# Optimization experiments

Hardware: AMD Instinct MI355X
Metric: run time of the kernel (lower is better)

## Reference

```python
import jax, jax.numpy as jnp
import numpy as np

HEAD_K_DIM = 128  # linear_key_head_dim (not derivable from weight shapes alone)
EPS_NORM = 1e-6


def _l2norm(x, eps=1e-6):
    return x * jax.lax.rsqrt(jnp.sum(x * x, axis=-1, keepdims=True) + eps)


def setup_inputs() -> dict:
    key = jax.random.key(0)
    ks = jax.random.split(key, 9)
    B, S, H = 2, 1024, 2048
    Hv, Hk, Dk, Dv, K = 32, 16, 128, 128, 4
    key_dim, value_dim = Hk * Dk, Hv * Dv
    C = 2 * key_dim + value_dim  # conv_dim = 8192
    s = 0.02
    return {
        "hidden_states": jax.random.normal(ks[0], (B, S, H), jnp.float32),
        "conv_state": jnp.zeros((B, C, K - 1), jnp.float32),
        "recurrent_state": jnp.zeros((B, Hv, Dk, Dv), jnp.float32),
        "W_qkv": (jax.random.normal(ks[1], (C, H)) * s).astype(jnp.float32),
        "W_z": (jax.random.normal(ks[2], (value_dim, H)) * s).astype(jnp.float32),
        "W_b": (jax.random.normal(ks[3], (Hv, H)) * s).astype(jnp.float32),
        "W_a": (jax.random.normal(ks[4], (Hv, H)) * s).astype(jnp.float32),
        "conv_w": (jax.random.normal(ks[5], (C, K)) * s).astype(jnp.float32),
        "dt_bias": jnp.ones((Hv,), jnp.float32),
        "A_log": jnp.log(jax.random.uniform(ks[6], (Hv,), jnp.float32, 1e-3, 16.0)),
        "norm_weight": jnp.ones((Dv,), jnp.float32),
        "W_out": (jax.random.normal(ks[7], (H, value_dim)) * s).astype(jnp.float32),
    }


def reference(hidden_states, conv_state, recurrent_state, W_qkv, W_z, W_b, W_a,
              conv_w, dt_bias, A_log, norm_weight, W_out):
    B, S, H = hidden_states.shape
    Hv = dt_bias.shape[0]
    Dv = norm_weight.shape[0]
    C, K = conv_w.shape
    value_dim = Hv * Dv
    key_dim = (C - value_dim) // 2
    Dk = HEAD_K_DIM
    Hk = key_dim // Dk

    # input projections
    mixed_qkv = jnp.einsum('bsh,ch->bcs', hidden_states, W_qkv)  # (B, C, S)
    z = hidden_states @ W_z.T                                    # (B, S, value_dim)
    b = hidden_states @ W_b.T                                    # (B, S, Hv)
    a = hidden_states @ W_a.T                                    # (B, S, Hv)

    # causal depthwise conv over time with cached prefix state
    padded = jnp.concatenate([conv_state, mixed_qkv], axis=-1)   # (B, C, K-1+S)
    conv_out = sum(padded[:, :, k:k + S] * conv_w[:, k][None, :, None]
                   for k in range(K))                            # (B, C, S)
    conv_state_new = padded[:, :, -(K - 1):]
    mixed = jnp.swapaxes(jax.nn.silu(conv_out), 1, 2)            # (B, S, C)

    q = mixed[..., :key_dim].reshape(B, S, Hk, Dk)
    k = mixed[..., key_dim:2 * key_dim].reshape(B, S, Hk, Dk)
    v = mixed[..., 2 * key_dim:].reshape(B, S, Hv, Dv)

    beta = jax.nn.sigmoid(b)                                     # (B, S, Hv)
    g = -jnp.exp(A_log) * jax.nn.softplus(a + dt_bias)           # (B, S, Hv)

    rep = Hv // Hk
    if rep > 1:
        q = jnp.repeat(q, rep, axis=2)
        k = jnp.repeat(k, rep, axis=2)

    scale = Dk ** (-0.5)
    q = _l2norm(q) * scale
    k = _l2norm(k)

    # time-leading for scan: (S, B, Hv, ...)
    qT, kT, vT = (jnp.moveaxis(x, 1, 0) for x in (q, k, v))
    gT, betaT = jnp.moveaxis(g, 1, 0), jnp.moveaxis(beta, 1, 0)

    def step(state, xs):
        q_t, k_t, v_t, g_t, beta_t = xs
        state = state * jnp.exp(g_t)[..., None, None]            # decay
        kv_mem = jnp.einsum('bhk,bhkv->bhv', k_t, state)         # read
        delta = (v_t - kv_mem) * beta_t[..., None]               # correction
        state = state + jnp.einsum('bhk,bhv->bhkv', k_t, delta)  # write
        out_t = jnp.einsum('bhk,bhkv->bhv', q_t, state)          # readout
        return state, out_t

    final_state, outs = jax.lax.scan(step, recurrent_state.astype(jnp.float32),
                                     (qT, kT, vT, gT, betaT))
    core = jnp.moveaxis(outs, 0, 1)                              # (B, S, Hv, Dv)

    # gated RMS norm per value head
    var = jnp.mean(core * core, axis=-1, keepdims=True)
    xn = core * jax.lax.rsqrt(var + EPS_NORM) * norm_weight
    gated = xn * jax.nn.silu(z.reshape(B, S, Hv, Dv))

    output = gated.reshape(B, S, value_dim) @ W_out.T            # (B, S, H)
    return output, conv_state_new, final_state
```

## Files before the change

### kernel.cpp

```cpp
#include <hip/hip_runtime.h>
#include <cstdint>
#include <cstddef>

#define B_ 2
#define S_ 1024
#define H_ 2048
#define HV_ 32
#define HK_ 16
#define DK_ 128
#define DV_ 128
#define CC_ 8192
#define KEYDIM_ 2048
#define VALDIM_ 4096
#define NC_ 16
#define CS_ 64
#define NBIG 12416
#define NBIGP 12544

typedef __attribute__((ext_vector_type(8))) short bf16x8;
typedef __attribute__((ext_vector_type(4))) float f32x4;

__device__ __forceinline__ ushort f2bf_rne(float x) {
  union { float f; uint32_t u; } c; c.f = x;
  uint32_t u = c.u + 0x7FFFu + ((c.u >> 16) & 1u);
  return (ushort)(u >> 16);
}

__device__ __forceinline__ void gld16(const void* g, void* l) {
  __builtin_amdgcn_global_load_lds(
      (const __attribute__((address_space(1))) void*)g,
      (__attribute__((address_space(3))) void*)l, 16, 0, 0);
}

__global__ void f2bf_kernel(const float* __restrict__ in, ushort* __restrict__ out, int n) {
  int i = (blockIdx.x * 256 + threadIdx.x) * 4;
  if (i >= n) return;
  float4 v = *(const float4*)(in + i);
  ushort4 o;
  o.x = f2bf_rne(v.x); o.y = f2bf_rne(v.y);
  o.z = f2bf_rne(v.z); o.w = f2bf_rne(v.w);
  *(ushort4*)(out + i) = o;
}

__global__ void wcat_kernel(const float* __restrict__ Wqkv, const float* __restrict__ Wz,
                            const float* __restrict__ Wb, const float* __restrict__ Wa,
                            ushort* __restrict__ out) {
  int i = (blockIdx.x * 256 + threadIdx.x) * 4;
  if (i >= NBIGP * H_) return;
  int n = i >> 11;
  int k = i & (H_ - 1);
  float4 v = make_float4(0.f, 0.f, 0.f, 0.f);
  if (n < 8192)       v = *(const float4*)(Wqkv + (size_t)n * H_ + k);
  else if (n < 12288) v = *(const float4*)(Wz + (size_t)(n - 8192) * H_ + k);
  else if (n < 12320) v = *(const float4*)(Wb + (size_t)(n - 12288) * H_ + k);
  else if (n < 12352) v = *(const float4*)(Wa + (size_t)(n - 12320) * H_ + k);
  ushort4 o;
  o.x = f2bf_rne(v.x); o.y = f2bf_rne(v.y);
  o.z = f2bf_rne(v.z); o.w = f2bf_rne(v.w);
  *(ushort4*)(out + i) = o;
}

#define MEMF() asm volatile("" ::: "memory")
#define VMW(n) asm volatile("s_waitcnt vmcnt(" #n ")" ::: "memory")
#define BARR() do { __builtin_amdgcn_s_barrier(); MEMF(); } while (0)

#define ST(P, SHM, RG, o, kq) do {                                  \
    gld16((P) + (kq),      &SHM[o][((RG) * 2 + 0) * 512]);          \
    gld16((P) + (kq) + 32, &SHM[o][((RG) * 2 + 1) * 512]);          \
  } while (0)

#define LDA(ah, c) do { _Pragma("unroll")                                            \
    for (int i_ = 0; i_ < 4; i_++) { _Pragma("unroll")                               \
      for (int h_ = 0; h_ < 2; h_++)                                                 \
        aF[i_ * 2 + h_] = *(const bf16x8*)(                                          \
            &sAm[c][((wm * 8 + (ah) * 4 + i_) * 2 + h_) * 512 + lane * 8]); } } while (0)

#define LDB(dst, bh, c) do { _Pragma("unroll")                                       \
    for (int j_ = 0; j_ < 2; j_++) { _Pragma("unroll")                               \
      for (int h_ = 0; h_ < 2; h_++)                                                 \
        dst[j_ * 2 + h_] = *(const bf16x8*)(                                         \
            &sBm[c][((wn * 4 + (bh) * 2 + j_) * 2 + h_) * 512 + lane * 8]); } } while (0)

#define MM(ah, bh, bsrc) do {                                                        \
    __builtin_amdgcn_s_setprio(1);                                                   \
    _Pragma("unroll") for (int h_ = 0; h_ < 2; h_++)                                 \
    _Pragma("unroll") for (int i_ = 0; i_ < 4; i_++)                                 \
    _Pragma("unroll") for (int j_ = 0; j_ < 2; j_++)                                 \
      acc[(ah) * 4 + i_][(bh) * 2 + j_] = __builtin_amdgcn_mfma_f32_16x16x32_bf16(   \
          aF[i_ * 2 + h_], bsrc[j_ * 2 + h_], acc[(ah) * 4 + i_][(bh) * 2 + j_],     \
          0, 0, 0);                                                                  \
    __builtin_amdgcn_s_setprio(0);                                                   \
  } while (0)

__global__ __launch_bounds__(512, 2) void gemm256_8ph(
    const ushort* __restrict__ A, const ushort* __restrict__ B,
    float* __restrict__ C, int Ns, int K)
{
  __shared__ ushort sAm[2][16384];
  __shared__ ushort sBm[2][16384];

  const int t = threadIdx.x;
  const int wave = t >> 6, lane = t & 63;
  const int wm = wave >> 2, wn = wave & 3;
  const int l15 = lane & 15, l4 = lane >> 4;
  const int mt = blockIdx.x, nt = blockIdx.y;

  const int rgS0 = (wave & 3) + (wave >> 2) * 8;
  const int rgS3 = rgS0 + 4;
  const int rgS1 = (wave & 1) + (wave >> 1) * 4;
  const int rgS2 = rgS1 + 2;

  const ushort* aP0 = A + (size_t)(mt * 256 + rgS0 * 16 + l15) * K + l4 * 8;
  const ushort* aP1 = A + (size_t)(mt * 256 + rgS3 * 16 + l15) * K + l4 * 8;
  const ushort* bP0 = B + (size_t)(nt * 256 + rgS1 * 16 + l15) * K + l4 * 8;
  const ushort* bP1 = B + (size_t)(nt * 256 + rgS2 * 16 + l15) * K + l4 * 8;

  f32x4 acc[8][4];
  #pragma unroll
  for (int i = 0; i < 8; i++)
    #pragma unroll
    for (int j = 0; j < 4; j++)
      #pragma unroll
      for (int r = 0; r < 4; r++) acc[i][j][r] = 0.f;

  bf16x8 aF[8], bF0[4], bF1[4];

  ST(aP0, sAm, rgS0, 0, 0); MEMF();
  ST(bP0, sBm, rgS1, 0, 0); MEMF();
  ST(bP1, sBm, rgS2, 0, 0); MEMF();
  ST(aP1, sAm, rgS3, 0, 0); MEMF();

  const int NT = K >> 6;
  for (int tt = 0; tt < NT - 1; tt++) {
    const int c = tt & 1, o = c ^ 1;
    const int kq = (tt + 1) << 6;
    VMW(4); BARR();
    ST(aP0, sAm, rgS0, o, kq);
    LDA(0, c); LDB(bF0, 0, c);
    MM(0, 0, bF0);
    VMW(4); BARR();
    ST(bP0, sBm, rgS1, o, kq);
    LDB(bF1, 1, c);
    MM(0, 1, bF1);
    VMW(4); BARR();
    ST(bP1, sBm, rgS2, o, kq);
    LDA(1, c);
    MM(1, 1, bF1);
    MEMF();
    ST(aP1, sAm, rgS3, o, kq);
    MM(1, 0, bF0);
  }
  {
    const int c = (NT - 1) & 1;
    VMW(4); BARR();
    LDA(0, c); LDB(bF0, 0, c);
    MM(0, 0, bF0);
    VMW(2); BARR();
    LDB(bF1, 1, c);
    MM(0, 1, bF1);
    VMW(0); BARR();
    LDA(1, c);
    MM(1, 1, bF1);
    MM(1, 0, bF0);
  }

  #pragma unroll
  for (int mf = 0; mf < 8; mf++) {
    const int row0 = mt * 256 + wm * 128 + mf * 16 + l4 * 4;
    #pragma unroll
    for (int nf = 0; nf < 4; nf++) {
      const int col = nt * 256 + wn * 64 + nf * 16 + l15;
      if (col < Ns) {
        #pragma unroll
        for (int r = 0; r < 4; r++)
          C[(size_t)(row0 + r) * Ns + col] = acc[mf][nf][r];
      }
    }
  }
}

__device__ __forceinline__ void stage_tile(
    const ushort* aS0, const ushort* aS1, const ushort* bS0, const ushort* bS1,
    ushort* ldsA, ushort* ldsB, int wave, int k0)
{
  #pragma unroll
  for (int h = 0; h < 2; h++) {
    gld16(aS0 + k0 + h * 32, ldsA + h * 4096 + (wave * 2 + 0) * 512);
    gld16(aS1 + k0 + h * 32, ldsA + h * 4096 + (wave * 2 + 1) * 512);
    gld16(bS0 + k0 + h * 32, ldsB + h * 4096 + (wave * 2 + 0) * 512);
    gld16(bS1 + k0 + h * 32, ldsB + h * 4096 + (wave * 2 + 1) * 512);
  }
}

__global__ __launch_bounds__(256) void gemm_bf16_nt(
    const ushort* __restrict__ A, const ushort* __restrict__ B,
    float* __restrict__ C, int M, int N, int K)
{
  __shared__ ushort sL[2][2][8192];
  int t = threadIdx.x;
  int wave = t >> 6, lane = t & 63;
  int wm = wave >> 1, wn = wave & 1;
  int lrow = lane & 15, quad = lane >> 4;
  int mt = blockIdx.x, nt = blockIdx.y;

  f32x4 acc[4][4];
  #pragma unroll
  for (int i = 0; i < 4; i++)
    #pragma unroll
    for (int j = 0; j < 4; j++)
      #pragma unroll
      for (int r = 0; r < 4; r++) acc[i][j][r] = 0.f;

  const ushort* aS0 = A + (size_t)(mt * 128 + (wave * 2 + 0) * 16 + lrow) * K + quad * 8;
  const ushort* aS1 = A + (size_t)(mt * 128 + (wave * 2 + 1) * 16 + lrow) * K + quad * 8;
  const ushort* bS0 = B + (size_t)(nt * 128 + (wave * 2 + 0) * 16 + lrow) * K + quad * 8;
  const ushort* bS1 = B + (size_t)(nt * 128 + (wave * 2 + 1) * 16 + lrow) * K + quad * 8;

  stage_tile(aS0, aS1, bS0, bS1, &sL[0][0][0], &sL[0][1][0], wave, 0);
  __syncthreads();

  const int NK = K >> 6;
  for (int it = 0; it < NK; it++) {
    if (it + 1 < NK)
      stage_tile(aS0, aS1, bS0, bS1,
                 &sL[(it + 1) & 1][0][0], &sL[(it + 1) & 1][1][0],
                 wave, (it + 1) * 64);
    const ushort* bufA = &sL[it & 1][0][0];
    const ushort* bufB = &sL[it & 1][1][0];
    #pragma unroll
    for (int h = 0; h < 2; h++) {
      bf16x8 af[4], bfr[4];
      #pragma unroll
      for (int i = 0; i < 4; i++)
        af[i] = *(const bf16x8*)(bufA + h * 4096 + (wm * 4 + i) * 512 + lane * 8);
      #pragma unroll
      for (int j = 0; j < 4; j++)
        bfr[j] = *(const bf16x8*)(bufB + h * 4096 + (wn * 4 + j) * 512 + lane * 8);
      #pragma unroll
      for (int i = 0; i < 4; i++)
        #pragma unroll
        for (int j = 0; j < 4; j++)
          acc[i][j] = __builtin_amdgcn_mfma_f32_16x16x32_bf16(af[i], bfr[j], acc[i][j], 0, 0, 0);
    }
    __syncthreads();
  }

  #pragma unroll
  for (int i = 0; i < 4; i++) {
    int m_base = mt * 128 + wm * 64 + i * 16 + quad * 4;
    #pragma unroll
    for (int j = 0; j < 4; j++) {
      int n = nt * 128 + wn * 64 + j * 16 + lrow;
      #pragma unroll
      for (int rr = 0; rr < 4; rr++)
        C[(size_t)(m_base + rr) * N + n] = acc[i][j][rr];
    }
  }
}

__global__ void convstate_kernel(const float* __restrict__ Cbig,
                                 float* __restrict__ out)
{
  int idx = blockIdx.x * blockDim.x + threadIdx.x;
  if (idx >= B_ * CC_ * 3) return;
  int j = idx % 3;
  int c = (idx / 3) % CC_;
  int b = idx / (3 * CC_);
  out[idx] = Cbig[((size_t)(b * S_ + (S_ - 3 + j))) * NBIG + c];
}

__global__ __launch_bounds__(128) void prep_qkv(
    const float* __restrict__ Cbig, const float* __restrict__ conv_state,
    const float* __restrict__ conv_w,
    float* __restrict__ Qn, float* __restrict__ Kn, float* __restrict__ Vb)
{
  int group = blockIdx.x, s = blockIdx.y, b = blockIdx.z;
  int t = threadIdx.x;
  int c = group * 128 + t;
  float acc = 0.f;
  #pragma unroll
  for (int kk = 0; kk < 4; kk++) {
    int sp = s - 3 + kk;
    float x = (sp < 0) ? conv_state[((size_t)(b * CC_ + c)) * 3 + (3 + sp)]
                       : Cbig[((size_t)(b * S_ + sp)) * NBIG + c];
    acc += conv_w[c * 4 + kk] * x;
  }
  float val = acc / (1.f + __expf(-acc));

  if (group < 32) {
    __shared__ float red2[2];
    float p = val * val;
    #pragma unroll
    for (int off = 32; off > 0; off >>= 1) p += __shfl_xor(p, off);
    if ((t & 63) == 0) red2[t >> 6] = p;
    __syncthreads();
    float r = rsqrtf(red2[0] + red2[1] + 1e-6f);
    if (group < 16) {
      r *= 0.08838834764831845f;
      Qn[(((size_t)(b * HK_ + group)) * S_ + s) * DK_ + t] = val * r;
    } else {
      Kn[(((size_t)(b * HK_ + (group - 16))) * S_ + s) * DK_ + t] = val * r;
    }
  } else {
    Vb[(((size_t)(b * HV_ + (group - 32))) * S_ + s) * DV_ + t] = val;
  }
}

__global__ void prep_gb(const float* __restrict__ Cbig,
                        const float* __restrict__ A_log, const float* __restrict__ dt_bias,
                        float* __restrict__ g_buf, float* __restrict__ beta_buf)
{
  int idx = blockIdx.x * blockDim.x + threadIdx.x;
  if (idx >= B_ * HV_ * S_) return;
  int s = idx & (S_ - 1);
  int hv = (idx >> 10) & 31;
  int b = idx >> 15;
  float bv = Cbig[((size_t)(b * S_ + s)) * NBIG + 12288 + hv];
  float av = Cbig[((size_t)(b * S_ + s)) * NBIG + 12320 + hv];
  float x = av + dt_bias[hv];
  float sp = (x > 20.f) ? x : log1pf(__expf(x));
  g_buf[idx] = -__expf(A_log[hv]) * sp;
  beta_buf[idx] = 1.f / (1.f + __expf(-bv));
}

__device__ __forceinline__ int swf4(int r, int f) { return r * 32 + (f ^ (r & 31)); }
__device__ __forceinline__ int swf1(int r, int k) {
  return r * 128 + 4 * ((k >> 2) ^ (r & 31)) + (k & 3);
}

__global__ __launch_bounds__(256) void cp_kernel(
    const float* __restrict__ Qn, const float* __restrict__ Kn,
    const float* __restrict__ Vb,
    const float* __restrict__ g_buf, const float* __restrict__ beta_buf,
    float* __restrict__ G_buf, float* __restrict__ M_buf,
    float* __restrict__ KcD, float* __restrict__ D0p)
{
  __shared__ float sK[64 * 128];
  __shared__ float sX[32 * 128];
  __shared__ float sT[64 * 64];
  float* sG  = sT;
  float* sBe = sT + 64;
  float* sA  = sX;
  float* tTw = sX;
  float* tTb = sX;
  float4* sK4 = (float4*)sK;
  float4* sX4 = (float4*)sX;

  const int ch = blockIdx.x;
  const int bh = ch / NC_, c = ch % NC_;
  const int b = bh >> 5, hv = bh & 31, hk = hv >> 1;
  const int s0 = c * CS_;
  const int t = threadIdx.x;
  const size_t gOff = (size_t)bh * S_ + s0;

  float Gw0 = 0.f, Bw0 = 0.f;
  if (t < 64) {
    float gi = g_buf[gOff + t];
    Gw0 = gi;
    #pragma unroll
    for (int off = 1; off < 64; off <<= 1) {
      float o = __shfl_up(Gw0, off);
      if (t >= off) Gw0 += o;
    }
    G_buf[gOff + t] = Gw0;
    sG[t] = Gw0;
    Bw0 = beta_buf[gOff + t];
    sBe[t] = Bw0;
  }
  {
    const float4* src = (const float4*)(Kn + ((size_t)(b * HK_ + hk) * S_ + s0) * DK_);
    #pragma unroll
    for (int u = 0; u < 8; u++) {
      int idx = u * 256 + t;
      sK4[swf4(idx >> 5, idx & 31)] = src[idx];
    }
  }
  __syncthreads();

  const float4* qsrc = (const float4*)(Qn + ((size_t)(b * HK_ + hk) * S_ + s0) * DK_);
  {
    int ti2 = t >> 4, tj = t & 15;
    for (int h = 0; h < 2; h++) {
      #pragma unroll
      for (int u = 0; u < 4; u++) {
        int idx = u * 256 + t;
        sX4[swf4(idx >> 5, idx & 31)] = qsrc[h * 1024 + idx];
      }
      __syncthreads();
      float accM[2][4];
      #pragma unroll
      for (int a = 0; a < 2; a++)
        #pragma unroll
        for (int e = 0; e < 4; e++) accM[a][e] = 0.f;
      for (int k4 = 0; k4 < 32; k4++) {
        float4 qv[2], kv[4];
        qv[0] = sX4[swf4(ti2, k4)];
        qv[1] = sX4[swf4(ti2 + 16, k4)];
        #pragma unroll
        for (int e = 0; e < 4; e++) kv[e] = sK4[swf4(tj + 16 * e, k4)];
        #pragma unroll
        for (int a = 0; a < 2; a++)
          #pragma unroll
          for (int e = 0; e < 4; e++)
            accM[a][e] += qv[a].x * kv[e].x + qv[a].y * kv[e].y +
                          qv[a].z * kv[e].z + qv[a].w * kv[e].w;
      }
      #pragma unroll
      for (int a = 0; a < 2; a++) {
        int iG = h * 32 + ti2 + 16 * a;
        float Gi = sG[iG];
        #pragma unroll
        for (int e = 0; e < 4; e++) {
          int j = tj + 16 * e;
          float m = (j <= iG) ? __expf(Gi - sG[j]) * accM[a][e] : 0.f;
          M_buf[(size_t)ch * 4096 + iG * 64 + j] = m;
        }
      }
      __syncthreads();
    }
  }

  {
    int ti = t >> 4, tj = t & 15;
    float accA[4][4];
    #pragma unroll
    for (int a = 0; a < 4; a++)
      #pragma unroll
      for (int e = 0; e < 4; e++) accA[a][e] = 0.f;
    for (int k4 = 0; k4 < 32; k4++) {
      float4 ki[4], kj[4];
      #pragma unroll
      for (int e = 0; e < 4; e++) {
        ki[e] = sK4[swf4(ti + 16 * e, k4)];
        kj[e] = sK4[swf4(tj + 16 * e, k4)];
      }
      #pragma unroll
      for (int a = 0; a < 4; a++)
        #pragma unroll
        for (int e = 0; e < 4; e++)
          accA[a][e] += ki[a].x * kj[e].x + ki[a].y * kj[e].y +
                        ki[a].z * kj[e].z + ki[a].w * kj[e].w;
    }
    float resA[4][4];
    #pragma unroll
    for (int a = 0; a < 4; a++) {
      int i = ti + 16 * a;
      float Gi = sG[i], Bi = sBe[i];
      #pragma unroll
      for (int e = 0; e < 4; e++) {
        int j = tj + 16 * e;
        resA[a][e] = (j < i) ? Bi * __expf(Gi - sG[j]) * accA[a][e] : 0.f;
      }
    }
    __syncthreads();
    #pragma unroll
    for (int a = 0; a < 4; a++)
      #pragma unroll
      for (int e = 0; e < 4; e++)
        sA[(ti + 16 * a) * 64 + (tj + 16 * e)] = resA[a][e];
  }
  __syncthreads();

  if (t < 64) {
    sT[t] = (t == 0) ? 1.f : 0.f;
    for (int i = 1; i < 64; i++) {
      float acc = 0.f;
      for (int j = 0; j < i; j++) acc += sA[i * 64 + j] * sT[j * 64 + t];
      sT[i * 64 + t] = ((t == i) ? 1.f : 0.f) - acc;
    }
    float w = Bw0 * __expf(Gw0);
    for (int j = 0; j < 64; j++) {
      float wj = __shfl(w, j);
      tTw[j * 64 + t] = sT[t * 64 + j] * wj;
    }
  }
  __syncthreads();

  {
    int i04 = t >> 4, tk = t & 15;
    float accK[4][8];
    #pragma unroll
    for (int r = 0; r < 4; r++)
      #pragma unroll
      for (int u = 0; u < 8; u++) accK[r][u] = 0.f;
    for (int j = 0; j < 64; j++) {
      float4 tw = ((float4*)tTw)[j * 16 + i04];
      #pragma unroll
      for (int u = 0; u < 8; u++) {
        float kv = sK[swf1(j, tk + 16 * u)];
        accK[0][u] += tw.x * kv; accK[1][u] += tw.y * kv;
        accK[2][u] += tw.z * kv; accK[3][u] += tw.w * kv;
      }
    }
    size_t base = (size_t)ch * NBIG;
    #pragma unroll
    for (int r = 0; r < 4; r++)
      #pragma unroll
      for (int u = 0; u < 8; u++)
        KcD[base + (i04 * 4 + r) * 128 + tk + 16 * u] = accK[r][u];
  }
  __syncthreads();

  if (t < 64) {
    for (int j = 0; j < 64; j++) {
      float bj = __shfl(Bw0, j);
      tTb[j * 64 + t] = sT[t * 64 + j] * bj;
    }
  }
  {
    const float4* src = (const float4*)(Vb + ((size_t)bh * S_ + s0) * DV_);
    #pragma unroll
    for (int u = 0; u < 8; u++) {
      int idx = u * 256 + t;
      sK4[swf4(idx >> 5, idx & 31)] = src[idx];
    }
  }
  __syncthreads();

  {
    int i04 = t >> 4, tv_ = t & 15;
    float accD[4][8];
    #pragma unroll
    for (int r = 0; r < 4; r++)
      #pragma unroll
      for (int u = 0; u < 8; u++) accD[r][u] = 0.f;
    for (int j = 0; j < 64; j++) {
      float4 tb = ((float4*)tTb)[j * 16 + i04];
      #pragma unroll
      for (int u = 0; u < 8; u++) {
        float vv = sK[swf1(j, tv_ + 16 * u)];
        accD[0][u] += tb.x * vv; accD[1][u] += tb.y * vv;
        accD[2][u] += tb.z * vv; accD[3][u] += tb.w * vv;
      }
    }
    size_t base = (size_t)ch * NBIG;
    #pragma unroll
    for (int r = 0; r < 4; r++)
      #pragma unroll
      for (int u = 0; u < 8; u++)
        D0p[base + (i04 * 4 + r) * 128 + tv_ + 16 * u] = accD[r][u];
  }
}

__global__ __launch_bounds__(256) void phaseb_kernel(
    const float* __restrict__ rec_state, const float* __restrict__ Qn,
    const float* __restrict__ Kn, const float* __restrict__ G_buf,
    float* __restrict__ KcD, const float* __restrict__ D0p,
    float* __restrict__ Oq_buf, float* __restrict__ final_state)
{
  __shared__ float sS[128 * 32];
  __shared__ float sKT[128 * 64];
  __shared__ float sQT[128 * 64];
  __shared__ float sD[64 * 32];

  const int blk = blockIdx.x;
  const int bh = (blk & 7) | ((blk >> 5) << 3);
  const int vq = (blk >> 3) & 3;
  const int b = bh >> 5, hv = bh & 31, hk = hv >> 1;
  const int t = threadIdx.x;
  const int vbase = vq * 32;
  const float* gG = G_buf + (size_t)bh * S_;

  #pragma unroll
  for (int u = 0; u < 4; u++) {
    int idx = u * 256 + t;
    int k = idx >> 3;
    int v4 = (idx & 7) * 4;
    *(float4*)(&sS[k * 32 + v4]) =
        *(const float4*)(&rec_state[((size_t)bh * 128 + k) * 128 + vbase + v4]);
  }
  __syncthreads();

  const int si = t & 63, skq = t >> 6;
  const int ti = t >> 3;
  const int tv = t & 7;
  const int tk = t >> 3;

  for (int c = 0; c < NC_; c++) {
    const size_t ch = (size_t)bh * NC_ + c;
    const int s0 = c * CS_;
    const float GC = gG[s0 + 63];
    const float eGC = __expf(GC);

    {
      float eGi = __expf(gG[s0 + si]);
      const float* kcRow = KcD + ch * NBIG + si * 128 + skq * 32;
      const float* qRow  = Qn + ((size_t)(b * HK_ + hk) * S_ + s0 + si) * DK_ + skq * 32;
      #pragma unroll
      for (int u = 0; u < 8; u++) {
        float4 kc = *(const float4*)(kcRow + u * 4);
        float4 qv = *(const float4*)(qRow + u * 4);
        int kk = skq * 32 + u * 4;
        sKT[(kk + 0) * 64 + si] = kc.x; sKT[(kk + 1) * 64 + si] = kc.y;
        sKT[(kk + 2) * 64 + si] = kc.z; sKT[(kk + 3) * 64 + si] = kc.w;
        sQT[(kk + 0) * 64 + si] = qv.x * eGi; sQT[(kk + 1) * 64 + si] = qv.y * eGi;
        sQT[(kk + 2) * 64 + si] = qv.z * eGi; sQT[(kk + 3) * 64 + si] = qv.w * eGi;
      }
    }
    __syncthreads();

    {
      float accD[2][4], accO[2][4];
      #pragma unroll
      for (int r = 0; r < 2; r++) {
        float4 d0 = *(const float4*)(&D0p[ch * NBIG + (size_t)(ti * 2 + r) * 128 + vbase + tv * 4]);
        accD[r][0] = d0.x; accD[r][1] = d0.y; accD[r][2] = d0.z; accD[r][3] = d0.w;
        accO[r][0] = accO[r][1] = accO[r][2] = accO[r][3] = 0.f;
      }
      for (int k = 0; k < 128; k++) {
        float2 kc = *(const float2*)(&sKT[k * 64 + ti * 2]);
        float2 qb = *(const float2*)(&sQT[k * 64 + ti * 2]);
        float4 sv = *(const float4*)(&sS[k * 32 + tv * 4]);
        accD[0][0] -= kc.x * sv.x; accD[0][1] -= kc.x * sv.y;
        accD[0][2] -= kc.x * sv.z; accD[0][3] -= kc.x * sv.w;
        accD[1][0] -= kc.y * sv.x; accD[1][1] -= kc.y * sv.y;
        accD[1][2] -= kc.y * sv.z; accD[1][3] -= kc.y * sv.w;
        accO[0][0] += qb.x * sv.x; accO[0][1] += qb.x * sv.y;
        accO[0][2] += qb.x * sv.z; accO[0][3] += qb.x * sv.w;
        accO[1][0] += qb.y * sv.x; accO[1][1] += qb.y * sv.y;
        accO[1][2] += qb.y * sv.z; accO[1][3] += qb.y * sv.w;
      }
      #pragma unroll
      for (int r = 0; r < 2; r++) {
        int i = ti * 2 + r;
        float4 dv = make_float4(accD[r][0], accD[r][1], accD[r][2], accD[r][3]);
        float4 ov = make_float4(accO[r][0], accO[r][1], accO[r][2], accO[r][3]);
        *(float4*)(&sD[i * 32 + tv * 4]) = dv;
        *(float4*)(&KcD[ch * NBIG + (size_t)i * 128 + vbase + tv * 4]) = dv;
        *(float4*)(&Oq_buf[ch * 8192 + (size_t)i * 128 + vbase + tv * 4]) = ov;
      }
    }
    __syncthreads();

    {
      float sc = __expf(GC - gG[s0 + si]);
      const float* kRow = Kn + ((size_t)(b * HK_ + hk) * S_ + s0 + si) * DK_ + skq * 32;
      #pragma unroll
      for (int u = 0; u < 8; u++) {
        float4 x = *(const float4*)(kRow + u * 4);
        x.x *= sc; x.y *= sc; x.z *= sc; x.w *= sc;
        int kg = skq * 8 + u;
        *(float4*)(&sKT[si * 128 + 4 * (kg ^ (si & 31))]) = x;
      }
    }
    __syncthreads();

    {
      float acc[4][4];
      #pragma unroll
      for (int r = 0; r < 4; r++)
        acc[r][0] = acc[r][1] = acc[r][2] = acc[r][3] = 0.f;
      for (int i = 0; i < 64; i++) {
        float4 d  = *(const float4*)(&sD[i * 32 + tv * 4]);
        float4 ka = *(const float4*)(&sKT[i * 128 + 4 * (tk ^ (i & 31))]);
        acc[0][0] += ka.x * d.x; acc[0][1] += ka.x * d.y;
        acc[0][2] += ka.x * d.z; acc[0][3] += ka.x * d.w;
        acc[1][0] += ka.y * d.x; acc[1][1] += ka.y * d.y;
        acc[1][2] += ka.y * d.z; acc[1][3] += ka.y * d.w;
        acc[2][0] += ka.z * d.x; acc[2][1] += ka.z * d.y;
        acc[2][2] += ka.z * d.z; acc[2][3] += ka.z * d.w;
        acc[3][0] += ka.w * d.x; acc[3][1] += ka.w * d.y;
        acc[3][2] += ka.w * d.z; acc[3][3] += ka.w * d.w;
      }
      #pragma unroll
      for (int r = 0; r < 4; r++) {
        int k = tk * 4 + r;
        float4 s = *(const float4*)(&sS[k * 32 + tv * 4]);
        s.x = s.x * eGC + acc[r][0]; s.y = s.y * eGC + acc[r][1];
        s.z = s.z * eGC + acc[r][2]; s.w = s.w * eGC + acc[r][3];
        *(float4*)(&sS[k * 32 + tv * 4]) = s;
      }
    }
    __syncthreads();
  }

  #pragma unroll
  for (int u = 0; u < 4; u++) {
    int idx = u * 256 + t;
    int k = idx >> 3;
    int v4 = (idx & 7) * 4;
    *(float4*)(&final_state[((size_t)bh * 128 + k) * 128 + vbase + v4]) =
        *(const float4*)(&sS[k * 32 + v4]);
  }
}

__global__ __launch_bounds__(128) void phasec_kernel(
    const float* __restrict__ KcD, const float* __restrict__ Oq_buf,
    const float* __restrict__ M_buf, const float* __restrict__ norm_weight,
    const float* __restrict__ Cbig, ushort* __restrict__ zg_bf)
{
  __shared__ float sM[4096];
  __shared__ float red[2][2];
  int ch = blockIdx.x;
  int bh = ch / NC_, c = ch % NC_;
  int b = bh >> 5, hv = bh & 31;
  int s0 = c * CS_;
  int v = threadIdx.x;

  float Dr[64];
  #pragma unroll
  for (int j = 0; j < 64; j++) Dr[j] = KcD[(size_t)ch * NBIG + j * 128 + v];
  {
    const float4* src = (const float4*)(M_buf + (size_t)ch * 4096);
    #pragma unroll
    for (int u = 0; u < 8; u++) ((float4*)sM)[u * 128 + v] = src[u * 128 + v];
  }
  __syncthreads();
  float nw = norm_weight[v];

  for (int i = 0; i < 64; i++) {
    float o = Oq_buf[(size_t)ch * 8192 + i * 128 + v];
    const float4* mr = (const float4*)(sM + i * 64);
    #pragma unroll
    for (int j4 = 0; j4 < 16; j4++) {
      float4 m = mr[j4];
      o += m.x * Dr[4 * j4] + m.y * Dr[4 * j4 + 1] +
           m.z * Dr[4 * j4 + 2] + m.w * Dr[4 * j4 + 3];
    }
    float p = o * o;
    #pragma unroll
    for (int off = 32; off > 0; off >>= 1) p += __shfl_xor(p, off);
    if ((v & 63) == 0) red[i & 1][v >> 6] = p;
    __syncthreads();
    float var = (red[i & 1][0] + red[i & 1][1]) * (1.f / 128.f);
    float xn = o * rsqrtf(var + 1e-6f) * nw;
    float zv = Cbig[((size_t)(b * S_ + s0 + i)) * NBIG + 8192 + hv * DV_ + v];
    zg_bf[((size_t)(b * S_ + s0 + i)) * VALDIM_ + hv * DV_ + v] =
        f2bf_rne(xn * (zv / (1.f + __expf(-zv))));
  }
}

extern "C" void kernel_launch(void* const* d_in, const int* in_sizes, int n_in,
                              void* d_out, int out_size, void* d_ws, size_t ws_size,
                              hipStream_t stream)
{
  const float* hs          = (const float*)d_in[0];
  const float* conv_state  = (const float*)d_in[1];
  const float* rec_state   = (const float*)d_in[2];
  const float* W_qkv       = (const float*)d_in[3];
  const float* W_z         = (const float*)d_in[4];
  const float* W_b         = (const float*)d_in[5];
  const float* W_a         = (const float*)d_in[6];
  const float* conv_w      = (const float*)d_in[7];
  const float* dt_bias     = (const float*)d_in[8];
  const float* A_log       = (const float*)d_in[9];
  const float* norm_weight = (const float*)d_in[10];
  const float* W_out       = (const float*)d_in[11];

  float* out       = (float*)d_out;
  float* out_conv  = out + (size_t)B_ * S_ * H_;
  float* out_state = out_conv + (size_t)B_ * CC_ * 3;

  float* ws = (float*)d_ws;
  float* Cbig = ws;
  float* KcD  = Cbig;
  float* D0p  = Cbig + (size_t)1024 * NBIG;
  float* g_buf    = ws + 25427968;
  float* beta_buf = ws + 25493504;
  float* G_buf    = ws + 25559040;
  float* Qn       = ws + 25624576;
  float* Kn       = ws + 29818880;
  float* Vb       = ws + 34013184;
  float* M_buf    = ws + 42401792;
  float* Oq_buf   = Vb;

  ushort* Wcat_bf = (ushort*)(ws + 25427968);
  ushort* hs_bf   = (ushort*)(ws + 38273024);
  ushort* zg_bf   = (ushort*)Qn;
  ushort* Wout_bf = (ushort*)Kn;

  const int M = B_ * S_;

  f2bf_kernel<<<(M * H_) / 1024, 256, 0, stream>>>(hs, hs_bf, M * H_);
  wcat_kernel<<<(NBIGP * H_) / 1024, 256, 0, stream>>>(W_qkv, W_z, W_b, W_a, Wcat_bf);
  gemm256_8ph<<<dim3(M / 256, NBIGP / 256), 512, 0, stream>>>(hs_bf, Wcat_bf, Cbig, NBIG, H_);
  convstate_kernel<<<(B_ * CC_ * 3 + 255) / 256, 256, 0, stream>>>(Cbig, out_conv);
  prep_qkv<<<dim3(64, S_, B_), 128, 0, stream>>>(Cbig, conv_state, conv_w, Qn, Kn, Vb);
  prep_gb<<<(B_ * HV_ * S_ + 255) / 256, 256, 0, stream>>>(Cbig, A_log, dt_bias, g_buf, beta_buf);
  cp_kernel<<<B_ * HV_ * NC_, 256, 0, stream>>>(Qn, Kn, Vb, g_buf, beta_buf,
                                                G_buf, M_buf, KcD, D0p);
  phaseb_kernel<<<B_ * HV_ * 4, 256, 0, stream>>>(rec_state, Qn, Kn, G_buf,
                                                  KcD, D0p, Oq_buf, out_state);
  f2bf_kernel<<<(H_ * VALDIM_) / 1024, 256, 0, stream>>>(W_out, Wout_bf, H_ * VALDIM_);
  phasec_kernel<<<B_ * HV_ * NC_, 128, 0, stream>>>(KcD, Oq_buf, M_buf,
                                                    norm_weight, Cbig, zg_bf);
  gemm_bf16_nt<<<dim3(M / 128, H_ / 128), 256, 0, stream>>>(zg_bf, Wout_bf, out, M, H_, VALDIM_);
}
```

Baseline: 952.9 us.

## Restructure GEMM main loop to prefetch A sub-tile two stages ahead

Reorders the double-buffered GEMM pipeline so the first A quarter-tile of the next-next K step is staged early, and LDS reads now come before the barriers and global-to-LDS stores. The epilogue iteration is folded into the main loop, with dummy loads at offset zero for out-of-range steps. The aim is to hide global load latency better and to shorten stalls between MFMA groups. In exchange it adds extra barriers per iteration and redundant loads in the final iterations.

```diff
diff --git a/kernel.cpp b/kernel.cpp
--- a/kernel.cpp
+++ b/kernel.cpp
@@ -129,40 +129,35 @@
   ST(bP0, sBm, rgS1, 0, 0); MEMF();
   ST(bP1, sBm, rgS2, 0, 0); MEMF();
   ST(aP1, sAm, rgS3, 0, 0); MEMF();
+  ST(aP0, sAm, rgS0, 1, 64); MEMF();
+  VMW(6); BARR();
 
   const int NT = K >> 6;
-  for (int tt = 0; tt < NT - 1; tt++) {
+  for (int tt = 0; tt < NT; tt++) {
     const int c = tt & 1, o = c ^ 1;
-    const int kq = (tt + 1) << 6;
+    const int kq1 = (tt + 1 < NT) ? (tt + 1) << 6 : 0;
+    const int kq2 = (tt + 2 < NT) ? (tt + 2) << 6 : 0;
+    LDA(0, c); LDB(bF0, 0, c);
     VMW(4); BARR();
-    ST(aP0, sAm, rgS0, o, kq);
-    LDA(0, c); LDB(bF0, 0, c);
+    ST(bP0, sBm, rgS1, o, kq1); MEMF();
     MM(0, 0, bF0);
+    BARR();
+    LDB(bF1, 1, c);
     VMW(4); BARR();
-    ST(bP0, sBm, rgS1, o, kq);
-    LDB(bF1, 1, c);
+    ST(bP1, sBm, rgS2, o, kq1); MEMF();
     MM(0, 1, bF1);
+    BARR();
+    LDA(1, c);
     VMW(4); BARR();
-    ST(bP1, sBm, rgS2, o, kq);
-    LDA(1, c);
+    ST(aP1, sAm, rgS3, o, kq1); MEMF();
     MM(1, 1, bF1);
-    MEMF();
-    ST(aP1, sAm, rgS3, o, kq);
+    BARR();
+    VMW(4); BARR();
+    ST(aP0, sAm, rgS0, c, kq2); MEMF();
     MM(1, 0, bF0);
-  }
-  {
-    const int c = (NT - 1) & 1;
-    VMW(4); BARR();
-    LDA(0, c); LDB(bF0, 0, c);
-    MM(0, 0, bF0);
-    VMW(2); BARR();
-    LDB(bF1, 1, c);
-    MM(0, 1, bF1);
-    VMW(0); BARR();
-    LDA(1, c);
-    MM(1, 1, bF1);
-    MM(1, 0, bF0);
-  }
+    BARR();
+  }
+  VMW(0);
 
   #pragma unroll
   for (int mf = 0; mf < 8; mf++) {
```

After: 942.2 us. No clear change (-1.1%).
